# Kernel optimization log

Measured on AMD Instinct MI355X. Metric: run time of the kernel, lower is better.

Reference implementation:

```python
import jax, jax.numpy as jnp
import numpy as np

HEADS = 16


def setup_inputs() -> dict:
    key = jax.random.key(0)
    ks = jax.random.split(key, 6)
    B, S, D = 2, 2048, 1024
    return {
        "x": jax.random.normal(ks[0], (B, S, D), dtype=jnp.float32),
        "q_in": jax.random.normal(ks[1], (B, S, D), dtype=jnp.float32),
        "WQ": jax.random.normal(ks[2], (D, D), dtype=jnp.float32) * 0.03,
        "WK": jax.random.normal(ks[3], (D, D), dtype=jnp.float32) * 0.03,
        "WV": jax.random.normal(ks[4], (D, D), dtype=jnp.float32) * 0.03,
        "WO": jax.random.normal(ks[5], (D, D), dtype=jnp.float32) * 0.03,
    }


def reference(x, q_in, WQ, WK, WV, WO):
    B, S, D = x.shape
    H = HEADS
    hd = D // H
    # projections; tf.split on last dim == reshape to (B,S,H,hd)
    Q = (q_in @ WQ).reshape(B, S, H, hd)
    K = (x @ WK).reshape(B, S, H, hd)
    V = (x @ WV).reshape(B, S, H, hd)
    scores = jnp.einsum("bqhd,bkhd->bhqk", Q, K)  # [B,H,S,S]
    # causal additive mask: 0 on/below diagonal, -inf above
    causal = jnp.tril(jnp.ones((S, S), dtype=bool))
    mask = jnp.where(causal, 0.0, -jnp.inf).astype(scores.dtype)
    # NOTE: original adds the mask BEFORE scaling, and scales by sqrt(d_model)
    attn = jax.nn.softmax((scores + mask) / np.sqrt(D).astype(scores.dtype), axis=-1)
    ctx = jnp.einsum("bhqk,bkhd->bqhd", attn, V).reshape(B, S, D)
    return ctx @ WO
```

## Files before the change

### kernel.cpp

```cpp
#include <hip/hip_runtime.h>


typedef __bf16 bf16_t;
typedef __attribute__((ext_vector_type(8))) __bf16 bf16x8;
typedef __attribute__((ext_vector_type(4))) __bf16 bf16x4;
typedef __attribute__((ext_vector_type(4))) float f32x4;

#define SCALE_LOG2E 0.045084220027780106f
#define FIXED_MAX 8.0f

__device__ __forceinline__ void async_load16(const void* g, void* l) {
  __builtin_amdgcn_global_load_lds(
      (const __attribute__((address_space(1))) void*)g,
      (__attribute__((address_space(3))) void*)l, 16, 0, 0);
}

__global__ void prep(const float* __restrict__ x, const float* __restrict__ q,
                     const float* __restrict__ w0, const float* __restrict__ w1,
                     const float* __restrict__ w2, const float* __restrict__ w3,
                     bf16_t* __restrict__ xb, bf16_t* __restrict__ qb,
                     bf16_t* __restrict__ wt) {
  const int bid = blockIdx.x;
  if (bid < 4096) {
    const float* src = (bid >= 2048) ? q : x;
    bf16_t* dst = (bid >= 2048) ? qb : xb;
    const size_t i = ((size_t)(bid & 2047) * 256 + threadIdx.x) * 8;
    float4 v0 = *(const float4*)(src + i);
    float4 v1 = *(const float4*)(src + i + 4);
    bf16x8 o;
    o[0] = (bf16_t)v0.x; o[1] = (bf16_t)v0.y; o[2] = (bf16_t)v0.z; o[3] = (bf16_t)v0.w;
    o[4] = (bf16_t)v1.x; o[5] = (bf16_t)v1.y; o[6] = (bf16_t)v1.z; o[7] = (bf16_t)v1.w;
    *(bf16x8*)(dst + i) = o;
  } else {
    const int wb = bid - 4096;
    const int z = wb >> 8;
    const float* W = z == 0 ? w0 : z == 1 ? w1 : z == 2 ? w2 : w3;
    bf16_t* dst = wt + (size_t)z * 1048576;
    const int r0 = ((wb >> 4) & 15) * 64, c0 = (wb & 15) * 64;
    __shared__ bf16_t t[64][72];
#pragma unroll
    for (int i = 0; i < 16; ++i) {
      int flat = i * 256 + threadIdx.x;
      int r = flat >> 6, c = flat & 63;
      t[c][r] = (bf16_t)W[(size_t)(r0 + r) * 1024 + c0 + c];
    }
    __syncthreads();
    const int c = threadIdx.x >> 2, seg = (threadIdx.x & 3) * 16;
    bf16x8 a = *(const bf16x8*)&t[c][seg];
    bf16x8 b = *(const bf16x8*)&t[c][seg + 8];
    bf16_t* drow = dst + (size_t)(c0 + c) * 1024 + r0 + seg;
    *(bf16x8*)drow = a;
    *(bf16x8*)(drow + 8) = b;
  }
}

template <int MODE>
__global__ __launch_bounds__(256, MODE == 2 ? 4 : 3) void gemm128(
    const bf16_t* __restrict__ Aq, const bf16_t* __restrict__ Ax,
    const bf16_t* __restrict__ Bt,
    bf16_t* __restrict__ Cq, bf16_t* __restrict__ Cvt, float* __restrict__ Cf) {
  constexpr int K = 1024;
  constexpr int NT = (MODE == 2) ? 2 : 4;
  constexpr int NROWS = NT * 32;
  const int n0 = blockIdx.x * NROWS;
  const int m0 = blockIdx.y * 128;
  const bf16_t* A = (MODE == 0 && n0 >= 1024) ? Ax : Aq;

  __shared__ bf16_t lA[128 * 32];
  __shared__ bf16_t lB[NROWS * 32];

  const int tid = threadIdx.x;
  const int w = tid >> 6, l = tid & 63;
  const int wm = (w & 1) * 64, wn = (w >> 1) * (NT * 16);
  const int sr = l >> 2;
  const int sk = (l & 3) * 8;
  const int fr = l & 15, fc = (l >> 4) * 8;

  f32x4 acc[4][NT] = {};

  for (int kt = 0; kt < K; kt += 32) {
    __syncthreads();
#pragma unroll
    for (int c = 0; c < 2; ++c) {
      const int ch = w * 2 + c;
      async_load16(A + (size_t)(m0 + ch * 16 + sr) * K + kt + sk, &lA[ch * 512]);
      if (NT == 4 || c == 0) {
        const int bch = (NT == 4) ? ch : w;
        async_load16(Bt + (size_t)(n0 + bch * 16 + sr) * K + kt + sk, &lB[bch * 512]);
      }
    }
    __syncthreads();
    bf16x8 af[4], bfr[NT];
#pragma unroll
    for (int i = 0; i < 4; ++i) af[i] = *(const bf16x8*)&lA[(wm + i * 16 + fr) * 32 + fc];
#pragma unroll
    for (int j = 0; j < NT; ++j) bfr[j] = *(const bf16x8*)&lB[(wn + j * 16 + fr) * 32 + fc];
#pragma unroll
    for (int i = 0; i < 4; ++i)
#pragma unroll
      for (int j = 0; j < NT; ++j)
        acc[i][j] = __builtin_amdgcn_mfma_f32_16x16x32_bf16(af[i], bfr[j], acc[i][j], 0, 0, 0);
  }

  if (MODE == 2) {
#pragma unroll
    for (int i = 0; i < 4; ++i) {
      const int m = m0 + wm + i * 16 + (l >> 4) * 4;
#pragma unroll
      for (int j = 0; j < NT; ++j) {
        const int n = n0 + wn + j * 16 + fr;
#pragma unroll
        for (int r = 0; r < 4; ++r) Cf[(size_t)(m + r) * 1024 + n] = acc[i][j][r];
      }
    }
  } else if (n0 < 2048) {
#pragma unroll
    for (int i = 0; i < 4; ++i) {
      const int m = m0 + wm + i * 16 + (l >> 4) * 4;
#pragma unroll
      for (int j = 0; j < NT; ++j) {
        const int n = n0 + wn + j * 16 + fr;
#pragma unroll
        for (int r = 0; r < 4; ++r) Cq[(size_t)(m + r) * 3072 + n] = (bf16_t)acc[i][j][r];
      }
    }
  } else {
#pragma unroll
    for (int i = 0; i < 4; ++i) {
      const int mb = m0 + wm + i * 16 + (l >> 4) * 4;
      const int bb = mb >> 11, ss = mb & 2047;
#pragma unroll
      for (int j = 0; j < NT; ++j) {
        const int nn = n0 - 2048 + wn + j * 16 + fr;
        const int hh = nn >> 6, dd = nn & 63;
        bf16x4 pk;
#pragma unroll
        for (int r = 0; r < 4; ++r) pk[r] = (bf16_t)acc[i][j][r];
        *(bf16x4*)(Cvt + (size_t)((bb * 16 + hh) * 64 + dd) * 2048 + ss) = pk;
      }
    }
  }
}

__global__ __launch_bounds__(512, 4) void attn8w(const bf16_t* __restrict__ qkv,
                                                 const bf16_t* __restrict__ vt,
                                                 bf16_t* __restrict__ ctx) {
  const int p = blockIdx.y;
  const int bh = blockIdx.x;
  const int b = bh >> 4, h = bh & 15;
  const int tid = threadIdx.x, w = tid >> 6, l = tid & 63;
  const int fr = l & 15, fq = l >> 4;
  const int qq4 = w & 3;
  const int kh = w >> 2;

  __shared__ __align__(16) bf16_t lK[2][64 * 64];
  __shared__ __align__(16) bf16_t lV[2][64 * 64];
  __shared__ __align__(16) bf16_t lP[8][16 * 40];
  __shared__ __align__(16) float lRed[4][16][68];

  const bf16_t* kg = qkv + (size_t)b * 2048 * 3072 + 1024 + h * 64;
  const bf16_t* vg = vt + (size_t)(b * 16 + h) * 64 * 2048;

  const int srow = l >> 3;
  const int swz = ((l & 7) ^ srow) * 8;
  const int xr = fr & 7;

  bf16x8 ones;
#pragma unroll
  for (int i = 0; i < 8; ++i) ones[i] = (bf16_t)1.0f;

#pragma unroll 1
  for (int phase = 0; phase < 2; ++phase) {
    const int qt = (phase == 0) ? (16 + p) : (15 - p);
    const int q0 = qt * 64;
    const int qw = q0 + qq4 * 16;

    bf16x8 qf[2];
#pragma unroll
    for (int ks = 0; ks < 2; ++ks)
      qf[ks] = *(const bf16x8*)(qkv + (size_t)(b * 2048 + qw + fr) * 3072 +
                                h * 64 + ks * 32 + fq * 8);

    f32x4 o[4] = {};
    f32x4 liacc = {};

    {
      const int row = w * 8 + srow;
      async_load16(kg + (size_t)row * 3072 + swz, &lK[0][w * 512]);
      async_load16(vg + (size_t)row * 2048 + swz, &lV[0][w * 512]);
    }

    for (int kt = 0; kt <= qt; ++kt) {
      const int buf = kt & 1;
      __syncthreads();
      if (kt < qt) {
        const int row = w * 8 + srow;
        async_load16(kg + (size_t)((kt + 1) * 64 + row) * 3072 + swz, &lK[buf ^ 1][w * 512]);
        async_load16(vg + (size_t)row * 2048 + (kt + 1) * 64 + swz, &lV[buf ^ 1][w * 512]);
      }

      const int kb = kt * 64 + kh * 32;
      if (kb > qw + 15) continue;

      f32x4 s[2] = {};
#pragma unroll
      for (int t = 0; t < 2; ++t)
#pragma unroll
        for (int ks = 0; ks < 2; ++ks) {
          bf16x8 kf = *(const bf16x8*)&lK[buf][(kh * 32 + t * 16 + fr) * 64 +
                                              ((ks * 4 + fq) ^ xr) * 8];
          s[t] = __builtin_amdgcn_mfma_f32_16x16x32_bf16(kf, qf[ks], s[t], 0, 0, 0);
        }

      const int qq = qw + fr;
      const bool needmask = (kb + 31) > qw;
#pragma unroll
      for (int t = 0; t < 2; ++t) {
        bf16x4 pk;
#pragma unroll
        for (int r = 0; r < 4; ++r) {
          float v = fmaf(s[t][r], SCALE_LOG2E, -FIXED_MAX);
          if (needmask && (kb + t * 16 + fq * 4 + r > qq)) v = -1e30f;
          pk[r] = (bf16_t)__builtin_amdgcn_exp2f(v);
        }
        *(bf16x4*)&lP[w][fr * 40 + t * 16 + fq * 4] = pk;
      }

      bf16x8 pf = *(const bf16x8*)&lP[w][fr * 40 + fq * 8];
#pragma unroll
      for (int dt = 0; dt < 4; ++dt) {
        bf16x8 vf = *(const bf16x8*)&lV[buf][(dt * 16 + fr) * 64 + ((kh * 4 + fq) ^ xr) * 8];
        o[dt] = __builtin_amdgcn_mfma_f32_16x16x32_bf16(vf, pf, o[dt], 0, 0, 0);
      }
      liacc = __builtin_amdgcn_mfma_f32_16x16x32_bf16(ones, pf, liacc, 0, 0, 0);
    }

    __syncthreads();
    if (kh) {
#pragma unroll
      for (int dt = 0; dt < 4; ++dt)
        *(f32x4*)&lRed[qq4][fr][dt * 16 + fq * 4] = o[dt];
      if (fq == 0) lRed[qq4][fr][64] = liacc[0];
    }
    __syncthreads();
    if (!kh) {
      const float lsum = liacc[0] + lRed[qq4][fr][64];
      const float inv = 1.f / lsum;
      bf16_t* cb = ctx + (size_t)(b * 2048 + qw + fr) * 1024 + h * 64;
#pragma unroll
      for (int dt = 0; dt < 4; ++dt) {
        f32x4 v = o[dt] + *(f32x4*)&lRed[qq4][fr][dt * 16 + fq * 4];
        bf16x4 ov;
#pragma unroll
        for (int r = 0; r < 4; ++r) ov[r] = (bf16_t)(v[r] * inv);
        *(bf16x4*)(cb + dt * 16 + fq * 4) = ov;
      }
    }
  }
}

extern "C" void kernel_launch(void* const* d_in, const int* in_sizes, int n_in,
                              void* d_out, int out_size, void* d_ws, size_t ws_size,
                              hipStream_t stream) {
  const float* x  = (const float*)d_in[0];
  const float* q  = (const float*)d_in[1];
  const float* WQ = (const float*)d_in[2];
  const float* WK = (const float*)d_in[3];
  const float* WV = (const float*)d_in[4];
  const float* WO = (const float*)d_in[5];
  float* out = (float*)d_out;

  bf16_t* qb  = (bf16_t*)d_ws;
  bf16_t* xb  = qb + 4194304;
  bf16_t* wt  = xb + 4194304;
  bf16_t* qkv = wt + 4194304;
  bf16_t* vtp = qkv + (size_t)4096 * 3072;
  bf16_t* ctx = vtp + 4194304;

  prep<<<dim3(5120), 256, 0, stream>>>(x, q, WQ, WK, WV, WO, xb, qb, wt);
  gemm128<0><<<dim3(24, 32), 256, 0, stream>>>(qb, xb, wt, qkv, vtp, nullptr);
  attn8w<<<dim3(32, 16), 512, 0, stream>>>(qkv, vtp, ctx);
  gemm128<2><<<dim3(16, 32), 256, 0, stream>>>(ctx, ctx, wt + (size_t)3072 * 1024,
                                               nullptr, nullptr, out);
}
```

Before: 188.3 us.

## Double GEMM K-tile to 64 with XOR-swizzled LDS and unroll attention double-buffer loop

The GEMM kernel now stages 64-wide K tiles, halving the number of barrier pairs per K sweep. It loads them with an XOR swizzle that matches the attention kernel's layout, to avoid LDS bank conflicts on the fragment reads. The attention kernel's K/V loop is manually unrolled by two with compile-time buffer indices and pointer increments, and per-thread LDS offsets are hoisted out of the loop. This doubles GEMM LDS use per block, which may reduce occupancy under the launch bounds.

```diff
diff --git a/kernel.cpp b/kernel.cpp
--- a/kernel.cpp
+++ b/kernel.cpp
@@ -66,46 +66,62 @@
   const int m0 = blockIdx.y * 128;
   const bf16_t* A = (MODE == 0 && n0 >= 1024) ? Ax : Aq;
 
-  __shared__ bf16_t lA[128 * 32];
-  __shared__ bf16_t lB[NROWS * 32];
+  __shared__ bf16_t lA[128 * 64];
+  __shared__ bf16_t lB[NROWS * 64];
 
   const int tid = threadIdx.x;
   const int w = tid >> 6, l = tid & 63;
   const int wm = (w & 1) * 64, wn = (w >> 1) * (NT * 16);
-  const int sr = l >> 2;
-  const int sk = (l & 3) * 8;
-  const int fr = l & 15, fc = (l >> 4) * 8;
+  const int fr = l & 15, fq = l >> 4;
+  const int xr = fr & 7;
+  const int srow = l >> 3;
+  const int swz = ((l & 7) ^ srow) * 8;
+
+  const int gk0 = (fq ^ xr) * 8;
+  const int gk1 = ((4 + fq) ^ xr) * 8;
 
   f32x4 acc[4][NT] = {};
 
-  for (int kt = 0; kt < K; kt += 32) {
-    __syncthreads();
-#pragma unroll
-    for (int c = 0; c < 2; ++c) {
-      const int ch = w * 2 + c;
-      async_load16(A + (size_t)(m0 + ch * 16 + sr) * K + kt + sk, &lA[ch * 512]);
-      if (NT == 4 || c == 0) {
-        const int bch = (NT == 4) ? ch : w;
-        async_load16(Bt + (size_t)(n0 + bch * 16 + sr) * K + kt + sk, &lB[bch * 512]);
-      }
-    }
-    __syncthreads();
-    bf16x8 af[4], bfr[NT];
-#pragma unroll
-    for (int i = 0; i < 4; ++i) af[i] = *(const bf16x8*)&lA[(wm + i * 16 + fr) * 32 + fc];
-#pragma unroll
-    for (int j = 0; j < NT; ++j) bfr[j] = *(const bf16x8*)&lB[(wn + j * 16 + fr) * 32 + fc];
+  for (int kt = 0; kt < K; kt += 64) {
+    __syncthreads();
+#pragma unroll
+    for (int c = 0; c < 4; ++c) {
+      const int ch = w * 4 + c;
+      async_load16(A + (size_t)(m0 + ch * 8 + srow) * K + kt + swz, &lA[ch * 512]);
+      if (NT == 4) {
+        async_load16(Bt + (size_t)(n0 + ch * 8 + srow) * K + kt + swz, &lB[ch * 512]);
+      } else if (c < 2) {
+        const int bch = w * 2 + c;
+        async_load16(Bt + (size_t)(n0 + bch * 8 + srow) * K + kt + swz, &lB[bch * 512]);
+      }
+    }
+    __syncthreads();
+    bf16x8 af[4][2], bfr[NT][2];
+#pragma unroll
+    for (int i = 0; i < 4; ++i) {
+      const int row = (wm + i * 16 + fr) * 64;
+      af[i][0] = *(const bf16x8*)&lA[row + gk0];
+      af[i][1] = *(const bf16x8*)&lA[row + gk1];
+    }
+#pragma unroll
+    for (int j = 0; j < NT; ++j) {
+      const int row = (wn + j * 16 + fr) * 64;
+      bfr[j][0] = *(const bf16x8*)&lB[row + gk0];
+      bfr[j][1] = *(const bf16x8*)&lB[row + gk1];
+    }
 #pragma unroll
     for (int i = 0; i < 4; ++i)
 #pragma unroll
-      for (int j = 0; j < NT; ++j)
-        acc[i][j] = __builtin_amdgcn_mfma_f32_16x16x32_bf16(af[i], bfr[j], acc[i][j], 0, 0, 0);
+      for (int j = 0; j < NT; ++j) {
+        acc[i][j] = __builtin_amdgcn_mfma_f32_16x16x32_bf16(af[i][0], bfr[j][0], acc[i][j], 0, 0, 0);
+        acc[i][j] = __builtin_amdgcn_mfma_f32_16x16x32_bf16(af[i][1], bfr[j][1], acc[i][j], 0, 0, 0);
+      }
   }
 
   if (MODE == 2) {
 #pragma unroll
     for (int i = 0; i < 4; ++i) {
-      const int m = m0 + wm + i * 16 + (l >> 4) * 4;
+      const int m = m0 + wm + i * 16 + fq * 4;
 #pragma unroll
       for (int j = 0; j < NT; ++j) {
         const int n = n0 + wn + j * 16 + fr;
@@ -116,7 +132,7 @@
   } else if (n0 < 2048) {
 #pragma unroll
     for (int i = 0; i < 4; ++i) {
-      const int m = m0 + wm + i * 16 + (l >> 4) * 4;
+      const int m = m0 + wm + i * 16 + fq * 4;
 #pragma unroll
       for (int j = 0; j < NT; ++j) {
         const int n = n0 + wn + j * 16 + fr;
@@ -127,7 +143,7 @@
   } else {
 #pragma unroll
     for (int i = 0; i < 4; ++i) {
-      const int mb = m0 + wm + i * 16 + (l >> 4) * 4;
+      const int mb = m0 + wm + i * 16 + fq * 4;
       const int bb = mb >> 11, ss = mb & 2047;
 #pragma unroll
       for (int j = 0; j < NT; ++j) {
@@ -165,6 +181,14 @@
   const int swz = ((l & 7) ^ srow) * 8;
   const int xr = fr & 7;
 
+  const int kbase = (kh * 32 + fr) * 64;
+  const int g0 = (fq ^ xr) * 8, g1 = ((4 + fq) ^ xr) * 8;
+  const int vbase = fr * 64;
+  const int vg0 = ((kh * 4 + fq) ^ xr) * 8;
+  const int pwr = fr * 40 + fq * 4;
+  const int prd = fr * 40 + fq * 8;
+  bf16_t* lPw = &lP[w][0];
+
   bf16x8 ones;
 #pragma unroll
   for (int i = 0; i < 8; ++i) ones[i] = (bf16_t)1.0f;
@@ -172,8 +196,7 @@
 #pragma unroll 1
   for (int phase = 0; phase < 2; ++phase) {
     const int qt = (phase == 0) ? (16 + p) : (15 - p);
-    const int q0 = qt * 64;
-    const int qw = q0 + qq4 * 16;
+    const int qw = qt * 64 + qq4 * 16;
 
     bf16x8 qf[2];
 #pragma unroll
@@ -184,34 +207,28 @@
     f32x4 o[4] = {};
     f32x4 liacc = {};
 
-    {
-      const int row = w * 8 + srow;
-      async_load16(kg + (size_t)row * 3072 + swz, &lK[0][w * 512]);
-      async_load16(vg + (size_t)row * 2048 + swz, &lV[0][w * 512]);
-    }
-
-    for (int kt = 0; kt <= qt; ++kt) {
-      const int buf = kt & 1;
-      __syncthreads();
-      if (kt < qt) {
-        const int row = w * 8 + srow;
-        async_load16(kg + (size_t)((kt + 1) * 64 + row) * 3072 + swz, &lK[buf ^ 1][w * 512]);
-        async_load16(vg + (size_t)row * 2048 + (kt + 1) * 64 + swz, &lV[buf ^ 1][w * 512]);
-      }
-
+    const bf16_t* kp = kg + (size_t)(w * 8 + srow) * 3072 + swz;
+    const bf16_t* vp = vg + (size_t)(w * 8 + srow) * 2048 + swz;
+
+    if (phase == 1) __syncthreads();
+    async_load16(kp, &lK[0][w * 512]);
+    async_load16(vp, &lV[0][w * 512]);
+    kp += 64 * 3072;
+    vp += 64;
+
+    auto compute = [&](int kt, int buf) {
       const int kb = kt * 64 + kh * 32;
-      if (kb > qw + 15) continue;
-
+      if (kb > qw + 15) return;
+      const bf16_t* lKb = &lK[buf][0];
+      const bf16_t* lVb = &lV[buf][0];
       f32x4 s[2] = {};
 #pragma unroll
-      for (int t = 0; t < 2; ++t)
-#pragma unroll
-        for (int ks = 0; ks < 2; ++ks) {
-          bf16x8 kf = *(const bf16x8*)&lK[buf][(kh * 32 + t * 16 + fr) * 64 +
-                                              ((ks * 4 + fq) ^ xr) * 8];
-          s[t] = __builtin_amdgcn_mfma_f32_16x16x32_bf16(kf, qf[ks], s[t], 0, 0, 0);
-        }
-
+      for (int t = 0; t < 2; ++t) {
+        bf16x8 k0 = *(const bf16x8*)&lKb[kbase + t * 1024 + g0];
+        bf16x8 k1 = *(const bf16x8*)&lKb[kbase + t * 1024 + g1];
+        s[t] = __builtin_amdgcn_mfma_f32_16x16x32_bf16(k0, qf[0], s[t], 0, 0, 0);
+        s[t] = __builtin_amdgcn_mfma_f32_16x16x32_bf16(k1, qf[1], s[t], 0, 0, 0);
+      }
       const int qq = qw + fr;
       const bool needmask = (kb + 31) > qw;
 #pragma unroll
@@ -223,16 +240,36 @@
           if (needmask && (kb + t * 16 + fq * 4 + r > qq)) v = -1e30f;
           pk[r] = (bf16_t)__builtin_amdgcn_exp2f(v);
         }
-        *(bf16x4*)&lP[w][fr * 40 + t * 16 + fq * 4] = pk;
-      }
-
-      bf16x8 pf = *(const bf16x8*)&lP[w][fr * 40 + fq * 8];
+        *(bf16x4*)&lPw[pwr + t * 16] = pk;
+      }
+      bf16x8 pf = *(const bf16x8*)&lPw[prd];
 #pragma unroll
       for (int dt = 0; dt < 4; ++dt) {
-        bf16x8 vf = *(const bf16x8*)&lV[buf][(dt * 16 + fr) * 64 + ((kh * 4 + fq) ^ xr) * 8];
+        bf16x8 vf = *(const bf16x8*)&lVb[vbase + dt * 1024 + vg0];
         o[dt] = __builtin_amdgcn_mfma_f32_16x16x32_bf16(vf, pf, o[dt], 0, 0, 0);
       }
       liacc = __builtin_amdgcn_mfma_f32_16x16x32_bf16(ones, pf, liacc, 0, 0, 0);
+    };
+
+    int kt = 0;
+#pragma unroll 1
+    while (true) {
+      __syncthreads();
+      if (kt < qt) {
+        async_load16(kp, &lK[1][w * 512]);
+        async_load16(vp, &lV[1][w * 512]);
+        kp += 64 * 3072; vp += 64;
+      }
+      compute(kt, 0);
+      if (++kt > qt) break;
+      __syncthreads();
+      if (kt < qt) {
+        async_load16(kp, &lK[0][w * 512]);
+        async_load16(vp, &lV[0][w * 512]);
+        kp += 64 * 3072; vp += 64;
+      }
+      compute(kt, 1);
+      if (++kt > qt) break;
     }
 
     __syncthreads();
```

Measured after the change: 182.8 us. -2.9%, faster.
